# Optimization experiments

Measured on AMD Instinct MI355X. Metric: run time of the kernel, lower is better.

The kernel has to match this reference:

```python
import jax, jax.numpy as jnp
from jax import lax
import numpy as np

B, N, S, K = 8, 4096, 1024, 32
D_FEAT = 64
EPS = 1e-5


def fps_idx(pts, npoint):
    # pts: [N,3] -> farthest point sampling indices [npoint] (deterministic start at 0)
    n = pts.shape[0]
    def body(i, state):
        dist, far, idxs = state
        idxs = idxs.at[i].set(far)
        d = jnp.sum((pts - pts[far]) ** 2, axis=-1)
        dist = jnp.minimum(dist, d)
        return dist, jnp.argmax(dist).astype(jnp.int32), idxs
    init = (jnp.full((n,), 1e10, pts.dtype), jnp.int32(0), jnp.zeros((npoint,), jnp.int32))
    _, _, idxs = lax.fori_loop(0, npoint, body, init)
    return idxs


def bn(x, g, b, axes, c_axis):
    # batch-norm, training mode (batch statistics), matching torch default module state
    m = jnp.mean(x, axes, keepdims=True)
    v = jnp.var(x, axes, keepdims=True)
    shape = [1] * x.ndim
    shape[c_axis] = -1
    return g.reshape(shape) * (x - m) * lax.rsqrt(v + EPS) + b.reshape(shape)


def conv1x1(x, w, b):
    # x: [B,C,S,K], w: [O,C], b: [O]
    return jnp.einsum('oc,bcsk->bosk', w, x) + b[None, :, None, None]


def setup_inputs():
    key = jax.random.key(0)
    ks = jax.random.split(key, 20)
    p = lambda k, shape: jax.random.normal(k, shape, jnp.float32) * 0.05
    inp = {
        'xyz': jax.random.normal(ks[0], (B, 3, N), jnp.float32),
        'features': jax.random.normal(ks[1], (B, D_FEAT, N), jnp.float32),
        # main MLP: 67 -> 64 -> 64 -> 128
        'w0': p(ks[2], (64, 67)), 'b0': p(ks[3], (64,)), 'g0': jnp.ones(64), 'be0': jnp.zeros(64),
        'w1': p(ks[4], (64, 64)), 'b1': p(ks[5], (64,)), 'g1': jnp.ones(64), 'be1': jnp.zeros(64),
        'w2': p(ks[6], (128, 64)), 'b2': p(ks[7], (128,)), 'g2': jnp.ones(128), 'be2': jnp.zeros(128),
        # WeightNet: 3 -> 8 -> 8 -> 16
        'ww0': p(ks[8], (8, 3)), 'wb0': p(ks[9], (8,)), 'wg0': jnp.ones(8), 'wbe0': jnp.zeros(8),
        'ww1': p(ks[10], (8, 8)), 'wb1': p(ks[11], (8,)), 'wg1': jnp.ones(8), 'wbe1': jnp.zeros(8),
        'ww2': p(ks[12], (16, 8)), 'wb2': p(ks[13], (16,)), 'wg2': jnp.ones(16), 'wbe2': jnp.zeros(16),
        # final linear 16*128 -> 128 and BN1d
        'lw': p(ks[14], (128, 16 * 128)), 'lb': p(ks[15], (128,)),
        'lg': jnp.ones(128), 'lbe': jnp.zeros(128),
    }
    return inp


def reference(xyz, features, w0, b0, g0, be0, w1, b1, g1, be1, w2, b2, g2, be2,
              ww0, wb0, wg0, wbe0, ww1, wb1, wg1, wbe1, ww2, wb2, wg2, wbe2,
              lw, lb, lg, lbe):
    xyz_t = jnp.transpose(xyz, (0, 2, 1))          # [B,N,3]
    feat_t = jnp.transpose(features, (0, 2, 1))    # [B,N,D]

    # farthest point sampling (indices non-differentiable, as in CUDA FPS)
    fidx = jax.vmap(lambda pts: fps_idx(pts, S))(lax.stop_gradient(xyz_t))  # [B,S]
    fps_xyz = jnp.take_along_axis(xyz_t, fidx[..., None], axis=1)           # [B,S,3]

    # KNN: squared distances [B,S,N], take K smallest
    d2 = (jnp.sum(fps_xyz ** 2, -1, keepdims=True)
          + jnp.sum(xyz_t ** 2, -1)[:, None, :]
          - 2.0 * jnp.einsum('bsc,bnc->bsn', fps_xyz, xyz_t))
    _, idx = lax.top_k(-lax.stop_gradient(d2), K)                            # [B,S,K]

    gather = jax.vmap(lambda src, i: src[i])
    grouped_xyz = gather(xyz_t, idx) - fps_xyz[:, :, None, :]                # [B,S,K,3]
    grouped_feat = gather(feat_t, idx)                                       # [B,S,K,D]
    nf = jnp.concatenate([grouped_xyz, grouped_feat], axis=-1)               # [B,S,K,3+D]

    nf = jnp.transpose(nf, (0, 3, 1, 2))                                     # [B,C,S,K]
    for w, b, g, be in ((w0, b0, g0, be0), (w1, b1, g1, be1), (w2, b2, g2, be2)):
        nf = jax.nn.relu(bn(conv1x1(nf, w, b), g, be, (0, 2, 3), 1))

    gx = jnp.transpose(grouped_xyz, (0, 3, 1, 2))                            # [B,3,S,K]
    wts = gx
    for w, b, g, be in ((ww0, wb0, wg0, wbe0), (ww1, wb1, wg1, wbe1), (ww2, wb2, wg2, wbe2)):
        wts = jax.nn.relu(bn(conv1x1(wts, w, b), g, be, (0, 2, 3), 1))       # [B,16,S,K]

    agg = jnp.einsum('bdsk,bcsk->bsdc', nf, wts)                             # [B,S,128,16]
    agg = agg.reshape(agg.shape[0], agg.shape[1], -1)                        # [B,S,2048] (D outer, C inner)
    lin = agg @ lw.T + lb                                                    # [B,S,128]
    lin = jnp.transpose(lin, (0, 2, 1))                                      # [B,128,S]
    out_f = jax.nn.relu(bn(lin, lg, lbe, (0, 2), 1))

    new_xyz = jnp.transpose(fps_xyz, (0, 2, 1))                              # [B,3,S]
    return (new_xyz, out_f)
```

## Files before the change

kernel.cpp:

```cpp
#include <hip/hip_runtime.h>
#include <hip/hip_bf16.h>

#define BB 8
#define NN 4096
#define SS 1024
#define KK 32
#define PP (BB*SS*KK)

typedef unsigned long long u64;
typedef unsigned int u32;
typedef unsigned short u16;
typedef float f32x2 __attribute__((ext_vector_type(2)));

#define ST_Y0 0
#define ST_W0 64
#define ST_Y1 72
#define ST_W1 136
#define ST_Y2 144
#define ST_W2 272
#define ST_LIN 288

static __device__ __forceinline__ float bf2f(u32 u){ return __uint_as_float(u<<16); }
static __device__ __forceinline__ u16 f2bf(float f){ u32 u=__float_as_uint(f); return (u16)((u + 0x7FFFu + ((u>>16)&1u))>>16); }

static __device__ __forceinline__ f32x2 pk_add(f32x2 a, f32x2 b){
  f32x2 d; asm("v_pk_add_f32 %0, %1, %2" : "=v"(d) : "v"(a), "v"(b)); return d;
}
static __device__ __forceinline__ f32x2 pk_mul(f32x2 a, f32x2 b){
  f32x2 d; asm("v_pk_mul_f32 %0, %1, %2" : "=v"(d) : "v"(a), "v"(b)); return d;
}

static __device__ __forceinline__ uint4 pack8(const float* v){
  uint4 r;
  r.x=(u32)f2bf(v[0])|((u32)f2bf(v[1])<<16);
  r.y=(u32)f2bf(v[2])|((u32)f2bf(v[3])<<16);
  r.z=(u32)f2bf(v[4])|((u32)f2bf(v[5])<<16);
  r.w=(u32)f2bf(v[6])|((u32)f2bf(v[7])<<16);
  return r;
}

static __device__ __forceinline__ void unp8_aff(uint4 r, const float* A, const float* C, int cb, float* o){
  o[0]=fmaxf(fmaf(bf2f(r.x&0xffffu),A[cb+0],C[cb+0]),0.f);
  o[1]=fmaxf(fmaf(bf2f(r.x>>16)    ,A[cb+1],C[cb+1]),0.f);
  o[2]=fmaxf(fmaf(bf2f(r.y&0xffffu),A[cb+2],C[cb+2]),0.f);
  o[3]=fmaxf(fmaf(bf2f(r.y>>16)    ,A[cb+3],C[cb+3]),0.f);
  o[4]=fmaxf(fmaf(bf2f(r.z&0xffffu),A[cb+4],C[cb+4]),0.f);
  o[5]=fmaxf(fmaf(bf2f(r.z>>16)    ,A[cb+5],C[cb+5]),0.f);
  o[6]=fmaxf(fmaf(bf2f(r.w&0xffffu),A[cb+6],C[cb+6]),0.f);
  o[7]=fmaxf(fmaf(bf2f(r.w>>16)    ,A[cb+7],C[cb+7]),0.f);
}

template<int CTRL, int RMASK>
static __device__ __forceinline__ u32 dppmax(u32 m){
  u32 t=(u32)__builtin_amdgcn_update_dpp(0, (int)m, CTRL, RMASK, 0xf, false);
  return t>m ? t : m;
}
template<int CTRL, int RMASK>
static __device__ __forceinline__ float dppadd1(float v){
  float t=__uint_as_float((u32)__builtin_amdgcn_update_dpp(0,(int)__float_as_uint(v),CTRL,RMASK,0xf,false));
  return v+t;
}
static __device__ __forceinline__ float dppsum(float v){
  v=dppadd1<0x111,0xf>(v);
  v=dppadd1<0x112,0xf>(v);
  v=dppadd1<0x114,0xf>(v);
  v=dppadd1<0x118,0xf>(v);
  v=dppadd1<0x142,0xa>(v);
  v=dppadd1<0x143,0xc>(v);
  return v;
}
static __device__ __forceinline__ float rl63(float v){
  return __uint_as_float((u32)__builtin_amdgcn_readlane((int)__float_as_uint(v),63));
}

__global__ __launch_bounds__(256) void k_featT(const float* __restrict__ f, float* __restrict__ ft,
    const float* __restrict__ w0,const float* __restrict__ w1,const float* __restrict__ w2,
    const float* __restrict__ ww0,const float* __restrict__ ww1,const float* __restrict__ ww2,
    float* __restrict__ w0t,float* __restrict__ w1t,float* __restrict__ w2t,
    float* __restrict__ wt0,float* __restrict__ wt1,float* __restrict__ wt2,
    float* __restrict__ statsf){
  __shared__ float tile[64][65];
  if (blockIdx.x==512){
    int t=threadIdx.x;
    for (int i=t;i<1024;i+=256) statsf[i]=0.f;
    for (int i=t;i<64*67;i+=256){ int o=i/67,k=i%67; w0t[k*64+o]=w0[i]; }
    for (int i=t;i<64*64;i+=256){ int o=i>>6,k=i&63; w1t[k*64+o]=w1[i]; }
    for (int i=t;i<128*64;i+=256){ int o=i>>6,k=i&63; w2t[k*128+o]=w2[i]; }
    for (int i=t;i<8*3;i+=256){ int o=i/3,k=i%3; wt0[k*8+o]=ww0[i]; }
    for (int i=t;i<8*8;i+=256){ int o=i>>3,k=i&7; wt1[k*8+o]=ww1[i]; }
    for (int i=t;i<16*8;i+=256){ int o=i>>3,k=i&7; wt2[k*16+o]=ww2[i]; }
    return;
  }
  int b=blockIdx.x>>6; int n0=(blockIdx.x&63)*64;
  const float* fb=f+(size_t)b*64*NN;
  int c0=threadIdx.x>>6, nn=threadIdx.x&63;
  #pragma unroll
  for (int it=0;it<16;it++){ int c=c0+it*4; tile[c][nn]=fb[(size_t)c*NN+n0+nn]; }
  __syncthreads();
  int cc=threadIdx.x&63, n1=threadIdx.x>>6;
  float* fo=ft+((size_t)b*NN+n0)*64;
  #pragma unroll
  for (int it=0;it<16;it++){ int n=n1+it*4; fo[(size_t)n*64+cc]=tile[cc][n]; }
}

__global__ __launch_bounds__(512) void k_fps(const float* __restrict__ xyz,
                                             float* __restrict__ fpsq, float* __restrict__ outx){
  __shared__ float X[NN], Y[NN], Z[NN];
  __shared__ float QX[SS], QY[SS], QZ[SS];
  __shared__ u64 red[2][8];
  int b=blockIdx.x, t=threadIdx.x;
  const float* xb=xyz+(size_t)b*3*NN;
  for (int i=t;i<NN;i+=512){ X[i]=xb[i]; Y[i]=xb[NN+i]; Z[i]=xb[2*NN+i]; }
  __syncthreads();
  f32x2 px[4],py[4],pz[4],dd[4];
  #pragma unroll
  for (int k=0;k<4;k++){
    int i=t*8+2*k;
    px[k].x=X[i]; px[k].y=X[i+1];
    py[k].x=Y[i]; py[k].y=Y[i+1];
    pz[k].x=Z[i]; pz[k].y=Z[i+1];
    dd[k].x=1e10f; dd[k].y=1e10f;
  }
  int wv=t>>6, ln=t&63;
  int far=0;
  for (int s=0;s<SS;s++){
    float fx=X[far], fy=Y[far], fz=Z[far];
    if (t==0){ QX[s]=fx; QY[s]=fy; QZ[s]=fz; }
    f32x2 nfx, nfy, nfz;
    nfx.x=-fx; nfx.y=-fx; nfy.x=-fy; nfy.y=-fy; nfz.x=-fz; nfz.y=-fz;
    #pragma unroll
    for (int k=0;k<4;k++){
      f32x2 dx=pk_add(px[k],nfx);
      f32x2 xx=pk_mul(dx,dx);
      f32x2 dy=pk_add(py[k],nfy);
      f32x2 yy=pk_mul(dy,dy);
      f32x2 dz=pk_add(pz[k],nfz);
      f32x2 zz=pk_mul(dz,dz);
      f32x2 s1=pk_add(xx,yy);
      f32x2 d2=pk_add(s1,zz);
      dd[k].x=fminf(dd[k].x,d2.x);
      dd[k].y=fminf(dd[k].y,d2.y);
    }
    float m01=fmaxf(dd[0].x,dd[0].y), m23=fmaxf(dd[1].x,dd[1].y);
    float m45=fmaxf(dd[2].x,dd[2].y), m67=fmaxf(dd[3].x,dd[3].y);
    u32 m=__float_as_uint(fmaxf(fmaxf(m01,m23),fmaxf(m45,m67)));
    m=dppmax<0x111,0xf>(m);
    m=dppmax<0x112,0xf>(m);
    m=dppmax<0x114,0xf>(m);
    m=dppmax<0x118,0xf>(m);
    u32 r15=(u32)__builtin_amdgcn_readlane((int)m,15);
    u32 r31=(u32)__builtin_amdgcn_readlane((int)m,31);
    u32 r47=(u32)__builtin_amdgcn_readlane((int)m,47);
    u32 r63=(u32)__builtin_amdgcn_readlane((int)m,63);
    u32 ab = r15>r31 ? r15 : r31;
    u32 cd = r47>r63 ? r47 : r63;
    u32 wmax = ab>cd ? ab : cd;
    int lj=8;
    if (__float_as_uint(dd[3].y)==wmax) lj=7;
    if (__float_as_uint(dd[3].x)==wmax) lj=6;
    if (__float_as_uint(dd[2].y)==wmax) lj=5;
    if (__float_as_uint(dd[2].x)==wmax) lj=4;
    if (__float_as_uint(dd[1].y)==wmax) lj=3;
    if (__float_as_uint(dd[1].x)==wmax) lj=2;
    if (__float_as_uint(dd[0].y)==wmax) lj=1;
    if (__float_as_uint(dd[0].x)==wmax) lj=0;
    u64 ball=__ballot(lj<8);
    u32 wl=(u32)__builtin_ctzll(ball);
    int gi=t*8+lj;
    u32 widx=(u32)__builtin_amdgcn_readlane(gi,wl);
    int pb=s&1;
    if (ln==0) red[pb][wv]=((u64)wmax<<32)|(u32)(4095u-widx);
    __syncthreads();
    const double* rd=(const double*)&red[pb][0];
    double g=fmax(fmax(fmax(rd[0],rd[1]),fmax(rd[2],rd[3])),
                  fmax(fmax(rd[4],rd[5]),fmax(rd[6],rd[7])));
    far=4095-(int)(__double_as_longlong(g)&0xFFFull);
  }
  __syncthreads();
  for (int i=t;i<SS;i+=512){
    float qx=QX[i], qy=QY[i], qz=QZ[i];
    float* q=&fpsq[((size_t)b*SS+i)*3]; q[0]=qx; q[1]=qy; q[2]=qz;
    outx[b*3*SS+i]=qx; outx[b*3*SS+SS+i]=qy; outx[b*3*SS+2*SS+i]=qz;
  }
}

#define KSTR 68
__global__ __launch_bounds__(256) void k_knn(const float* __restrict__ xyz, const float* __restrict__ fpsq,
                                             int* __restrict__ kidx){
  extern __shared__ char smem[];
  float* xs=(float*)smem;
  float* ys=xs+64*KSTR;
  float* zs=ys+64*KSTR;
  float* pn=zs+64*KSTR;
  int blk=blockIdx.x; int b=blk>>8; int s0=(blk&255)*4;
  const float* xb=xyz+(size_t)b*3*NN;
  for (int i=threadIdx.x;i<NN;i+=256){
    float x=xb[i],y=xb[NN+i],z=xb[2*NN+i];
    int slot=(i>>6)*KSTR+(i&63);
    xs[slot]=x; ys[slot]=y; zs[slot]=z;
    pn[slot]=__fadd_rn(__fadd_rn(__fmul_rn(x,x),__fmul_rn(y,y)),__fmul_rn(z,z));
  }
  __syncthreads();
  int wv=threadIdx.x>>6, ln=threadIdx.x&63;
  int s=s0+wv;
  const float* q=&fpsq[((size_t)b*SS+s)*3];
  float qx=q[0],qy=q[1],qz=q[2];
  float qn=__fadd_rn(__fadd_rn(__fmul_rn(qx,qx),__fmul_rn(qy,qy)),__fmul_rn(qz,qz));
  f32x2 qxx,qyy,qzz,qnn,mtwo;
  qxx.x=qx;qxx.y=qx; qyy.x=qy;qyy.y=qy; qzz.x=qz;qzz.y=qz; qnn.x=qn;qnn.y=qn;
  mtwo.x=-2.f; mtwo.y=-2.f;
  const float4* Xp=(const float4*)(xs+ln*KSTR);
  const float4* Yp=(const float4*)(ys+ln*KSTR);
  const float4* Zp=(const float4*)(zs+ln*KSTR);
  const float4* Pp=(const float4*)(pn+ln*KSTR);
  int base=ln*64;
  u64 v[64];
  #pragma unroll
  for (int g=0;g<16;g++){
    float4 x4=Xp[g], y4=Yp[g], z4=Zp[g], p4=Pp[g];
    #pragma unroll
    for (int h=0;h<2;h++){
      f32x2 px2,py2,pz2,pn2;
      if (h==0){ px2.x=x4.x;px2.y=x4.y; py2.x=y4.x;py2.y=y4.y; pz2.x=z4.x;pz2.y=z4.y; pn2.x=p4.x;pn2.y=p4.y; }
      else     { px2.x=x4.z;px2.y=x4.w; py2.x=y4.z;py2.y=y4.w; pz2.x=z4.z;pz2.y=z4.w; pn2.x=p4.z;pn2.y=p4.w; }
      f32x2 m1=pk_mul(qxx,px2);
      f32x2 mm=pk_mul(qyy,py2);
      f32x2 a1=pk_add(m1,mm);
      f32x2 m3=pk_mul(qzz,pz2);
      f32x2 dt=pk_add(a1,m3);
      f32x2 qp=pk_add(qnn,pn2);
      f32x2 nd=pk_mul(dt,mtwo);
      f32x2 d2=pk_add(qp,nd);
      #pragma unroll
      for (int e=0;e<2;e++){
        u32 bu=__float_as_uint(e?d2.y:d2.x);
        bu = ((int)bu<0)? ~bu : (bu|0x80000000u);
        v[g*4+h*2+e]=((u64)bu<<32)|(u32)(base+g*4+h*2+e);
      }
    }
  }
  u64 cand[8];
  #pragma unroll
  for (int gg=0;gg<8;gg++){
    u64 c=v[gg*8];
    #pragma unroll
    for (int j=1;j<8;j++){ u64 x=v[gg*8+j]; c = x<c?x:c; }
    cand[gg]=c;
  }
  u64 best=cand[0];
  #pragma unroll
  for (int gg=1;gg<8;gg++){ u64 x=cand[gg]; best = x<best?x:best; }
  int my=0;
  #pragma unroll 1
  for (int r=0;r<KK;r++){
    u64 w=best;
    #pragma unroll
    for (int m=1;m<64;m<<=1){ u64 o=__shfl_xor(w,m,64); w = o<w?o:w; }
    if (ln==r) my=(int)(w&0xFFFull);
    if (best==w){
      #pragma unroll
      for (int gg=0;gg<8;gg++){
        if (cand[gg]==w){
          u64 c=~0ull;
          #pragma unroll
          for (int j=0;j<8;j++){ u64 x=v[gg*8+j]; x = x>w ? x : ~0ull; c = x<c?x:c; }
          cand[gg]=c;
        }
      }
      u64 nb=cand[0];
      #pragma unroll
      for (int gg=1;gg<8;gg++){ u64 x=cand[gg]; nb = x<nb?x:nb; }
      best=nb;
    }
  }
  if (ln<KK) kidx[(((size_t)b*SS+s)<<5)+ln]=my;
}

__global__ __launch_bounds__(256) void k_l0(const float* __restrict__ xyz, const float* __restrict__ ft,
    const float* __restrict__ fpsq, const int* __restrict__ kidx,
    const float* __restrict__ w0t, const float* __restrict__ wt0,
    u16* __restrict__ y0, float* __restrict__ wl0, float* __restrict__ statsf){
  __shared__ u16 ytile[256][64];
  __shared__ float pS[4][64], pQ[4][64];
  __shared__ float pWS[4][8], pWQ[4][8];
  int t=threadIdx.x; int wv=t>>6, ln=t&63;
  int p=blockIdx.x*256+t;
  int b=p>>15;
  int site=p>>5;
  int j=kidx[p];
  const float* xb=xyz+(size_t)b*3*NN;
  const float* q=fpsq+(size_t)site*3;
  float gx=xb[j]-q[0], gy=xb[NN+j]-q[1], gz=xb[2*NN+j]-q[2];
  float acc[64];
  #pragma unroll
  for (int c=0;c<64;c++) acc[c]=fmaf(gx,w0t[c],fmaf(gy,w0t[64+c],gz*w0t[128+c]));
  const float4* fr=(const float4*)(ft+((size_t)b*NN+j)*64);
  #pragma unroll 1
  for (int kb=0;kb<4;kb++){
    float4 r0=fr[kb*4+0], r1=fr[kb*4+1], r2=fr[kb*4+2], r3=fr[kb*4+3];
    float ch[16]={r0.x,r0.y,r0.z,r0.w,r1.x,r1.y,r1.z,r1.w,r2.x,r2.y,r2.z,r2.w,r3.x,r3.y,r3.z,r3.w};
    const float* wb=w0t+(3+kb*16)*64;
    #pragma unroll
    for (int kk=0;kk<16;kk++){
      #pragma unroll
      for (int c=0;c<64;c++) acc[c]=fmaf(ch[kk],wb[kk*64+c],acc[c]);
    }
  }
  u16* yr=y0+(size_t)p*64;
  #pragma unroll
  for (int c8=0;c8<8;c8++){
    uint4 pk=pack8(&acc[c8*8]);
    ((uint4*)yr)[c8]=pk;
    *((uint4*)&ytile[t][c8*8])=pk;
  }
  float wa[8];
  #pragma unroll
  for (int o=0;o<8;o++) wa[o]=fmaf(gx,wt0[o],fmaf(gy,wt0[8+o],gz*wt0[16+o]));
  float4* wr=(float4*)(wl0+(size_t)p*8);
  wr[0]=make_float4(wa[0],wa[1],wa[2],wa[3]);
  wr[1]=make_float4(wa[4],wa[5],wa[6],wa[7]);
  float wS[8],wQ[8];
  #pragma unroll
  for (int o=0;o<8;o++){
    wS[o]=rl63(dppsum(wa[o]));
    wQ[o]=rl63(dppsum(wa[o]*wa[o]));
  }
  if (ln==0){
    #pragma unroll
    for (int o=0;o<8;o++){ pWS[wv][o]=wS[o]; pWQ[wv][o]=wQ[o]; }
  }
  __syncthreads();
  {
    int c=t&63, rg=t>>6;
    float S=0.f,Q=0.f;
    #pragma unroll 16
    for (int r=0;r<64;r++){
      float v=bf2f((u32)ytile[rg*64+r][c]);
      S+=v; Q=fmaf(v,v,Q);
    }
    pS[rg][c]=S; pQ[rg][c]=Q;
  }
  __syncthreads();
  if (t<64){
    float S=pS[0][t]+pS[1][t]+pS[2][t]+pS[3][t];
    float Q=pQ[0][t]+pQ[1][t]+pQ[2][t]+pQ[3][t];
    atomicAdd(&statsf[2*(ST_Y0+t)],S); atomicAdd(&statsf[2*(ST_Y0+t)+1],Q);
  } else if (t<72){
    int c=t-64;
    float S=pWS[0][c]+pWS[1][c]+pWS[2][c]+pWS[3][c];
    float Q=pWQ[0][c]+pWQ[1][c]+pWQ[2][c]+pWQ[3][c];
    atomicAdd(&statsf[2*(ST_W0+c)],S); atomicAdd(&statsf[2*(ST_W0+c)+1],Q);
  }
}

__global__ __launch_bounds__(256) void k_l1(const u16* __restrict__ y0, const float* __restrict__ wl0,
    const float* __restrict__ w1t, const float* __restrict__ wt1,
    const float* __restrict__ statsf,
    const float* __restrict__ g0v, const float* __restrict__ be0v,
    const float* __restrict__ wg0v, const float* __restrict__ wbe0v,
    u16* __restrict__ y1, float* __restrict__ wl1, float* __restrict__ statso){
  __shared__ float A0[64],C0[64],AW[8],CW[8];
  __shared__ u16 ytile[256][64];
  __shared__ float pS[4][64], pQ[4][64];
  __shared__ float pWS[4][8], pWQ[4][8];
  int t=threadIdx.x; int wv=t>>6, ln=t&63;
  if (t<64){
    float sm=statsf[(ST_Y0+t)*2], sq=statsf[(ST_Y0+t)*2+1];
    float mean=sm*(1.f/PP), var=fmaxf(sq*(1.f/PP)-mean*mean,0.f);
    float a=g0v[t]*rsqrtf(var+1e-5f); A0[t]=a; C0[t]=be0v[t]-mean*a;
  } else if (t<72){
    int c=t-64;
    float sm=statsf[(ST_W0+c)*2], sq=statsf[(ST_W0+c)*2+1];
    float mean=sm*(1.f/PP), var=fmaxf(sq*(1.f/PP)-mean*mean,0.f);
    float a=wg0v[c]*rsqrtf(var+1e-5f); AW[c]=a; CW[c]=wbe0v[c]-mean*a;
  }
  __syncthreads();
  int p=blockIdx.x*256+t;
  const uint4* yr=(const uint4*)(y0+(size_t)p*64);
  float acc[64];
  #pragma unroll
  for (int c=0;c<64;c++) acc[c]=0.f;
  #pragma unroll 1
  for (int kb=0;kb<4;kb++){
    uint4 r0=yr[kb*2], r1=yr[kb*2+1];
    float ch[16];
    unp8_aff(r0,A0,C0,kb*16,ch);
    unp8_aff(r1,A0,C0,kb*16+8,ch+8);
    const float* wb=w1t+kb*16*64;
    #pragma unroll
    for (int kk=0;kk<16;kk++){
      #pragma unroll
      for (int c=0;c<64;c++) acc[c]=fmaf(ch[kk],wb[kk*64+c],acc[c]);
    }
  }
  u16* yo=y1+(size_t)p*64;
  #pragma unroll
  for (int c8=0;c8<8;c8++){
    uint4 pk=pack8(&acc[c8*8]);
    ((uint4*)yo)[c8]=pk;
    *((uint4*)&ytile[t][c8*8])=pk;
  }
  const float4* wvp=(const float4*)(wl0+(size_t)p*8);
  float4 v0=wvp[0], v1=wvp[1];
  float wi[8]={v0.x,v0.y,v0.z,v0.w,v1.x,v1.y,v1.z,v1.w};
  float wo[8];
  #pragma unroll
  for (int o=0;o<8;o++) wo[o]=0.f;
  #pragma unroll
  for (int k=0;k<8;k++){
    float xr=fmaxf(fmaf(wi[k],AW[k],CW[k]),0.f);
    #pragma unroll
    for (int o=0;o<8;o++) wo[o]=fmaf(xr,wt1[k*8+o],wo[o]);
  }
  float4* wr=(float4*)(wl1+(size_t)p*8);
  wr[0]=make_float4(wo[0],wo[1],wo[2],wo[3]);
  wr[1]=make_float4(wo[4],wo[5],wo[6],wo[7]);
  float wS[8],wQ[8];
  #pragma unroll
  for (int o=0;o<8;o++){
    wS[o]=rl63(dppsum(wo[o]));
    wQ[o]=rl63(dppsum(wo[o]*wo[o]));
  }
  if (ln==0){
    #pragma unroll
    for (int o=0;o<8;o++){ pWS[wv][o]=wS[o]; pWQ[wv][o]=wQ[o]; }
  }
  __syncthreads();
  {
    int c=t&63, rg=t>>6;
    float S=0.f,Q=0.f;
    #pragma unroll 16
    for (int r=0;r<64;r++){
      float v=bf2f((u32)ytile[rg*64+r][c]);
      S+=v; Q=fmaf(v,v,Q);
    }
    pS[rg][c]=S; pQ[rg][c]=Q;
  }
  __syncthreads();
  if (t<64){
    float S=pS[0][t]+pS[1][t]+pS[2][t]+pS[3][t];
    float Q=pQ[0][t]+pQ[1][t]+pQ[2][t]+pQ[3][t];
    atomicAdd(&statso[2*(ST_Y1+t)],S); atomicAdd(&statso[2*(ST_Y1+t)+1],Q);
  } else if (t<72){
    int c=t-64;
    float S=pWS[0][c]+pWS[1][c]+pWS[2][c]+pWS[3][c];
    float Q=pWQ[0][c]+pWQ[1][c]+pWQ[2][c]+pWQ[3][c];
    atomicAdd(&statso[2*(ST_W1+c)],S); atomicAdd(&statso[2*(ST_W1+c)+1],Q);
  }
}

__global__ __launch_bounds__(256) void k_l2(const u16* __restrict__ y1, const float* __restrict__ wl1,
    const float* __restrict__ w2t, const float* __restrict__ wt2,
    const float* __restrict__ statsf,
    const float* __restrict__ g1v, const float* __restrict__ be1v,
    const float* __restrict__ wg1v, const float* __restrict__ wbe1v,
    u16* __restrict__ y2, float* __restrict__ wl2, float* __restrict__ statso){
  __shared__ float A1[64],C1[64],AW[8],CW[8];
  __shared__ u16 ytile[256][64];
  __shared__ float pS[4][64], pQ[4][64];
  __shared__ float pWS[4][16], pWQ[4][16];
  int t=threadIdx.x; int wv=t>>6, ln=t&63;
  if (t<64){
    float sm=statsf[(ST_Y1+t)*2], sq=statsf[(ST_Y1+t)*2+1];
    float mean=sm*(1.f/PP), var=fmaxf(sq*(1.f/PP)-mean*mean,0.f);
    float a=g1v[t]*rsqrtf(var+1e-5f); A1[t]=a; C1[t]=be1v[t]-mean*a;
  } else if (t<72){
    int c=t-64;
    float sm=statsf[(ST_W1+c)*2], sq=statsf[(ST_W1+c)*2+1];
    float mean=sm*(1.f/PP), var=fmaxf(sq*(1.f/PP)-mean*mean,0.f);
    float a=wg1v[c]*rsqrtf(var+1e-5f); AW[c]=a; CW[c]=wbe1v[c]-mean*a;
  }
  __syncthreads();
  int p=blockIdx.x*256+t;
  const uint4* yr=(const uint4*)(y1+(size_t)p*64);
  #pragma unroll 1
  for (int h=0;h<2;h++){
    float acc[64];
    #pragma unroll
    for (int c=0;c<64;c++) acc[c]=0.f;
    #pragma unroll 1
    for (int kb=0;kb<4;kb++){
      uint4 r0=yr[kb*2], r1=yr[kb*2+1];
      float ch[16];
      unp8_aff(r0,A1,C1,kb*16,ch);
      unp8_aff(r1,A1,C1,kb*16+8,ch+8);
      const float* wb=w2t+(size_t)kb*16*128+h*64;
      #pragma unroll
      for (int kk=0;kk<16;kk++){
        #pragma unroll
        for (int c=0;c<64;c++) acc[c]=fmaf(ch[kk],wb[kk*128+c],acc[c]);
      }
    }
    u16* yo=y2+(size_t)p*128+h*64;
    #pragma unroll
    for (int c8=0;c8<8;c8++){
      uint4 pk=pack8(&acc[c8*8]);
      ((uint4*)yo)[c8]=pk;
      *((uint4*)&ytile[t][c8*8])=pk;
    }
    __syncthreads();
    {
      int c=t&63, rg=t>>6;
      float S=0.f,Q=0.f;
      #pragma unroll 16
      for (int r=0;r<64;r++){
        float v=bf2f((u32)ytile[rg*64+r][c]);
        S+=v; Q=fmaf(v,v,Q);
      }
      pS[rg][c]=S; pQ[rg][c]=Q;
    }
    __syncthreads();
    if (t<64){
      float S=pS[0][t]+pS[1][t]+pS[2][t]+pS[3][t];
      float Q=pQ[0][t]+pQ[1][t]+pQ[2][t]+pQ[3][t];
      atomicAdd(&statso[2*(ST_Y2+h*64+t)],S); atomicAdd(&statso[2*(ST_Y2+h*64+t)+1],Q);
    }
    __syncthreads();
  }
  const float4* wvp=(const float4*)(wl1+(size_t)p*8);
  float4 v0=wvp[0], v1=wvp[1];
  float wi[8]={v0.x,v0.y,v0.z,v0.w,v1.x,v1.y,v1.z,v1.w};
  float wo[16];
  #pragma unroll
  for (int o=0;o<16;o++) wo[o]=0.f;
  #pragma unroll
  for (int k=0;k<8;k++){
    float xr=fmaxf(fmaf(wi[k],AW[k],CW[k]),0.f);
    #pragma unroll
    for (int o=0;o<16;o++) wo[o]=fmaf(xr,wt2[k*16+o],wo[o]);
  }
  float4* wr=(float4*)(wl2+(size_t)p*16);
  wr[0]=make_float4(wo[0],wo[1],wo[2],wo[3]);
  wr[1]=make_float4(wo[4],wo[5],wo[6],wo[7]);
  wr[2]=make_float4(wo[8],wo[9],wo[10],wo[11]);
  wr[3]=make_float4(wo[12],wo[13],wo[14],wo[15]);
  float wS[16],wQ[16];
  #pragma unroll
  for (int o=0;o<16;o++){
    wS[o]=rl63(dppsum(wo[o]));
    wQ[o]=rl63(dppsum(wo[o]*wo[o]));
  }
  if (ln==0){
    #pragma unroll
    for (int o=0;o<16;o++){ pWS[wv][o]=wS[o]; pWQ[wv][o]=wQ[o]; }
  }
  __syncthreads();
  if (t<16){
    float S=pWS[0][t]+pWS[1][t]+pWS[2][t]+pWS[3][t];
    float Q=pWQ[0][t]+pWQ[1][t]+pWQ[2][t]+pWQ[3][t];
    atomicAdd(&statso[2*(ST_W2+t)],S); atomicAdd(&statso[2*(ST_W2+t)+1],Q);
  }
}

__global__ __launch_bounds__(256) void k_agg(const u16* __restrict__ y2, const float* __restrict__ wl2,
    const float* __restrict__ statsf,
    const float* __restrict__ g2v, const float* __restrict__ be2v,
    const float* __restrict__ wg2v, const float* __restrict__ wbe2v,
    u16* __restrict__ agg){
  __shared__ float A2[128],C2[128],AW[16],CW[16];
  __shared__ float nf[32*128];
  __shared__ float wt[32*16];
  int site=blockIdx.x; int t=threadIdx.x;
  if (t<128){
    float sm=statsf[(ST_Y2+t)*2], sq=statsf[(ST_Y2+t)*2+1];
    float mean=sm*(1.f/PP), var=fmaxf(sq*(1.f/PP)-mean*mean,0.f);
    float a=g2v[t]*rsqrtf(var+1e-5f); A2[t]=a; C2[t]=be2v[t]-mean*a;
  } else if (t<144){
    int c=t-128;
    float sm=statsf[(ST_W2+c)*2], sq=statsf[(ST_W2+c)*2+1];
    float mean=sm*(1.f/PP), var=fmaxf(sq*(1.f/PP)-mean*mean,0.f);
    float a=wg2v[c]*rsqrtf(var+1e-5f); AW[c]=a; CW[c]=wbe2v[c]-mean*a;
  }
  __syncthreads();
  const uint4* src=(const uint4*)(y2+(size_t)site*32*128);
  #pragma unroll
  for (int it=0;it<2;it++){
    int idx=t+it*256;
    uint4 r=src[idx];
    int base=(idx*8)&127; int kq=(idx*8)>>7;
    unp8_aff(r,A2,C2,base,&nf[kq*128+base]);
  }
  #pragma unroll
  for (int it=0;it<2;it++){
    int i=t+it*256;
    float x=wl2[(size_t)site*512+i]; int c=i&15;
    wt[i]=fmaxf(fmaf(x,AW[c],CW[c]),0.f);
  }
  __syncthreads();
  int d=t>>1, cb=(t&1)*8;
  float acc[8];
  #pragma unroll
  for (int e=0;e<8;e++) acc[e]=0.f;
  #pragma unroll 4
  for (int kq=0;kq<32;kq++){
    float nv=nf[kq*128+d];
    #pragma unroll
    for (int e=0;e<8;e++) acc[e]=fmaf(nv,wt[kq*16+cb+e],acc[e]);
  }
  ((uint4*)(agg+(size_t)site*2048))[t]=pack8(acc);
}

__global__ __launch_bounds__(256) void k_lin(const u16* __restrict__ agg, const float* __restrict__ lw,
                                             float* __restrict__ lin, float* __restrict__ outst){
  __shared__ float As[32][33];
  __shared__ float Bs[32][128];
  __shared__ float stS[8][132], stQ[8][132];
  int s0=blockIdx.x*32; int t=threadIdx.x;
  int tx=t&31, ty=t>>5;
  float acc[4][4];
  #pragma unroll
  for (int i=0;i<4;i++){
    #pragma unroll
    for (int jj=0;jj<4;jj++) acc[i][jj]=0.f;
  }
  for (int kb=0;kb<2048;kb+=32){
    {
      int row=t>>3, kc=(t&7)*4;
      uint2 raw=*(const uint2*)(agg+((size_t)(s0+row))*2048+kb+kc);
      As[row][kc  ]=bf2f(raw.x&0xffffu); As[row][kc+1]=bf2f(raw.x>>16);
      As[row][kc+2]=bf2f(raw.y&0xffffu); As[row][kc+3]=bf2f(raw.y>>16);
    }
    {
      int o=t>>1, ks=(t&1)*16;
      const float* lr=lw+(size_t)o*2048+kb+ks;
      #pragma unroll
      for (int i=0;i<16;i+=4){
        float4 r=*(const float4*)(lr+i);
        Bs[ks+i][o]=r.x; Bs[ks+i+1][o]=r.y; Bs[ks+i+2][o]=r.z; Bs[ks+i+3][o]=r.w;
      }
    }
    __syncthreads();
    #pragma unroll 8
    for (int kk=0;kk<32;kk++){
      float av[4];
      #pragma unroll
      for (int i=0;i<4;i++) av[i]=As[ty*4+i][kk];
      float4 bv=*(const float4*)(&Bs[kk][tx*4]);
      #pragma unroll
      for (int i=0;i<4;i++){
        acc[i][0]=fmaf(av[i],bv.x,acc[i][0]);
        acc[i][1]=fmaf(av[i],bv.y,acc[i][1]);
        acc[i][2]=fmaf(av[i],bv.z,acc[i][2]);
        acc[i][3]=fmaf(av[i],bv.w,acc[i][3]);
      }
    }
    __syncthreads();
  }
  #pragma unroll
  for (int i=0;i<4;i++){
    float4 o4=make_float4(acc[i][0],acc[i][1],acc[i][2],acc[i][3]);
    *(float4*)(lin+((size_t)(s0+ty*4+i))*128+tx*4)=o4;
  }
  #pragma unroll
  for (int jj=0;jj<4;jj++){
    float a0=acc[0][jj],a1=acc[1][jj],a2=acc[2][jj],a3=acc[3][jj];
    stS[ty][tx*4+jj]=(a0+a1)+(a2+a3);
    stQ[ty][tx*4+jj]=fmaf(a3,a3,fmaf(a2,a2,fmaf(a1,a1,a0*a0)));
  }
  __syncthreads();
  if (t<128){
    float S=0.f,Q=0.f;
    #pragma unroll
    for (int k=0;k<8;k++){ S+=stS[k][t]; Q+=stQ[k][t]; }
    atomicAdd(&outst[2*t],S); atomicAdd(&outst[2*t+1],Q);
  }
}

__global__ __launch_bounds__(256) void k_out(const float* __restrict__ lin, const float* __restrict__ statsf,
    const float* __restrict__ lg, const float* __restrict__ lbe, float* __restrict__ outf){
  int t=blockIdx.x*256+threadIdx.x;
  int s4=(t&255)*4; int o=(t>>8)&127; int b=t>>15;
  float sm=statsf[(ST_LIN+o)*2], sq=statsf[(ST_LIN+o)*2+1];
  float mean=sm*(1.f/8192.f), var=fmaxf(sq*(1.f/8192.f)-mean*mean,0.f);
  float a=lg[o]*rsqrtf(var+1e-5f), cc=lbe[o]-mean*a;
  float v0=lin[((size_t)b*SS+s4+0)*128+o];
  float v1=lin[((size_t)b*SS+s4+1)*128+o];
  float v2=lin[((size_t)b*SS+s4+2)*128+o];
  float v3=lin[((size_t)b*SS+s4+3)*128+o];
  float4 r=make_float4(fmaxf(fmaf(v0,a,cc),0.f),fmaxf(fmaf(v1,a,cc),0.f),
                       fmaxf(fmaf(v2,a,cc),0.f),fmaxf(fmaf(v3,a,cc),0.f));
  *(float4*)(outf+((size_t)b*128+o)*SS+s4)=r;
}

extern "C" void kernel_launch(void* const* d_in, const int* in_sizes, int n_in,
                              void* d_out, int out_size, void* d_ws, size_t ws_size,
                              hipStream_t stream){
  (void)in_sizes;(void)n_in;(void)out_size;(void)ws_size;
  const float* xyz =(const float*)d_in[0];
  const float* feat=(const float*)d_in[1];
  const float* w0=(const float*)d_in[2];  const float* g0=(const float*)d_in[4];  const float* be0=(const float*)d_in[5];
  const float* w1=(const float*)d_in[6];  const float* g1=(const float*)d_in[8];  const float* be1=(const float*)d_in[9];
  const float* w2=(const float*)d_in[10]; const float* g2=(const float*)d_in[12]; const float* be2=(const float*)d_in[13];
  const float* ww0=(const float*)d_in[14]; const float* wg0=(const float*)d_in[16]; const float* wbe0=(const float*)d_in[17];
  const float* ww1=(const float*)d_in[18]; const float* wg1=(const float*)d_in[20]; const float* wbe1=(const float*)d_in[21];
  const float* ww2=(const float*)d_in[22]; const float* wg2=(const float*)d_in[24]; const float* wbe2=(const float*)d_in[25];
  const float* lw=(const float*)d_in[26]; const float* lg=(const float*)d_in[28]; const float* lbe=(const float*)d_in[29];
  float* out=(float*)d_out;
  char* ws=(char*)d_ws;

  size_t cur=0;
  auto alloc=[&](size_t bytes)->size_t{ cur=(cur+255)&~(size_t)255; size_t o=cur; cur+=bytes; return o; };
  size_t o_stats=alloc(4096);
  size_t o_w0t =alloc(67*64*4);
  size_t o_w1t =alloc(64*64*4);
  size_t o_w2t =alloc(64*128*4);
  size_t o_wt0 =alloc(3*8*4);
  size_t o_wt1 =alloc(8*8*4);
  size_t o_wt2 =alloc(8*16*4);
  size_t o_fpsq=alloc((size_t)BB*SS*3*4);
  size_t o_kidx=alloc((size_t)PP*4);
  size_t o_ft  =alloc((size_t)BB*NN*64*4);
  size_t o_y0  =alloc((size_t)PP*64*2);
  size_t o_y1  =alloc((size_t)PP*64*2);
  size_t o_y2  =alloc((size_t)PP*128*2);
  size_t o_wl0 =alloc((size_t)PP*8*4);
  size_t o_wl1 =alloc((size_t)PP*8*4);
  size_t o_wl2 =alloc((size_t)PP*16*4);
  size_t o_agg =alloc((size_t)8192*2048*2);
  size_t o_lin =alloc((size_t)8192*128*4);

  float* statsf=(float*)(ws+o_stats);
  float* w0t=(float*)(ws+o_w0t); float* w1t=(float*)(ws+o_w1t); float* w2t=(float*)(ws+o_w2t);
  float* wt0=(float*)(ws+o_wt0); float* wt1=(float*)(ws+o_wt1); float* wt2=(float*)(ws+o_wt2);
  float* fpsq=(float*)(ws+o_fpsq); int* kidx=(int*)(ws+o_kidx);
  float* ft=(float*)(ws+o_ft);
  u16* y0=(u16*)(ws+o_y0); u16* y1=(u16*)(ws+o_y1); u16* y2=(u16*)(ws+o_y2);
  float* wl0=(float*)(ws+o_wl0); float* wl1=(float*)(ws+o_wl1); float* wl2=(float*)(ws+o_wl2);
  u16* agg=(u16*)(ws+o_agg); float* lin=(float*)(ws+o_lin);

  size_t knn_smem = (size_t)4*64*KSTR*4;

  hipLaunchKernelGGL(k_featT,dim3(513),dim3(256),0,stream,feat,ft,
                     w0,w1,w2,ww0,ww1,ww2,w0t,w1t,w2t,wt0,wt1,wt2,statsf);
  hipLaunchKernelGGL(k_fps,dim3(BB),dim3(512),0,stream,xyz,fpsq,out);
  hipLaunchKernelGGL(k_knn,dim3(2048),dim3(256),knn_smem,stream,xyz,fpsq,kidx);
  hipLaunchKernelGGL(k_l0,dim3(PP/256),dim3(256),0,stream,xyz,ft,fpsq,kidx,w0t,wt0,y0,wl0,statsf);
  hipLaunchKernelGGL(k_l1,dim3(PP/256),dim3(256),0,stream,y0,wl0,w1t,wt1,statsf,g0,be0,wg0,wbe0,y1,wl1,statsf);
  hipLaunchKernelGGL(k_l2,dim3(PP/256),dim3(256),0,stream,y1,wl1,w2t,wt2,statsf,g1,be1,wg1,wbe1,y2,wl2,statsf);
  hipLaunchKernelGGL(k_agg,dim3(8192),dim3(256),0,stream,y2,wl2,statsf,g2,be2,wg2,wbe2,agg);
  hipLaunchKernelGGL(k_lin,dim3(256),dim3(256),0,stream,agg,lw,lin,statsf+2*ST_LIN);
  hipLaunchKernelGGL(k_out,dim3(1024),dim3(256),0,stream,lin,statsf,lg,lbe,out+BB*3*SS);
}
```

Baseline: 1.308 ms.

## Merge feature transpose and weight prep into FPS kernel to overlap with FPS

Fuses the feature-transpose/weight-transpose kernel into the FPS kernel launch. Blocks 0-7 run FPS, blocks 8-263 transpose feature tiles (two tiles per 512-thread block), and block 264 zeroes stats and transposes weights. Shared memory is a union of the FPS arrays and the transpose tiles. This hides the transpose work under the latency-bound serial FPS loop and removes one launch, but every block now reserves the larger FPS shared-memory footprint, which may limit how many transpose blocks run at once.

```diff
diff --git a/kernel.cpp b/kernel.cpp
--- a/kernel.cpp
+++ b/kernel.cpp
@@ -73,42 +73,47 @@
   return __uint_as_float((u32)__builtin_amdgcn_readlane((int)__float_as_uint(v),63));
 }
 
-__global__ __launch_bounds__(256) void k_featT(const float* __restrict__ f, float* __restrict__ ft,
+__global__ __launch_bounds__(512) void k_fps_ft(const float* __restrict__ xyz,
+    float* __restrict__ fpsq, float* __restrict__ outx,
+    const float* __restrict__ f, float* __restrict__ ft,
     const float* __restrict__ w0,const float* __restrict__ w1,const float* __restrict__ w2,
     const float* __restrict__ ww0,const float* __restrict__ ww1,const float* __restrict__ ww2,
     float* __restrict__ w0t,float* __restrict__ w1t,float* __restrict__ w2t,
     float* __restrict__ wt0,float* __restrict__ wt1,float* __restrict__ wt2,
     float* __restrict__ statsf){
-  __shared__ float tile[64][65];
-  if (blockIdx.x==512){
-    int t=threadIdx.x;
-    for (int i=t;i<1024;i+=256) statsf[i]=0.f;
-    for (int i=t;i<64*67;i+=256){ int o=i/67,k=i%67; w0t[k*64+o]=w0[i]; }
-    for (int i=t;i<64*64;i+=256){ int o=i>>6,k=i&63; w1t[k*64+o]=w1[i]; }
-    for (int i=t;i<128*64;i+=256){ int o=i>>6,k=i&63; w2t[k*128+o]=w2[i]; }
-    for (int i=t;i<8*3;i+=256){ int o=i/3,k=i%3; wt0[k*8+o]=ww0[i]; }
-    for (int i=t;i<8*8;i+=256){ int o=i>>3,k=i&7; wt1[k*8+o]=ww1[i]; }
-    for (int i=t;i<16*8;i+=256){ int o=i>>3,k=i&7; wt2[k*16+o]=ww2[i]; }
+  __shared__ union USm {
+    struct { float X[NN],Y[NN],Z[NN]; float QX[SS],QY[SS],QZ[SS]; u64 red[2][8]; } a;
+    float tile[2][64][65];
+  } sm;
+  int blk=blockIdx.x; int t=threadIdx.x;
+  if (blk>=8){
+    if (blk==264){
+      for (int i=t;i<1024;i+=512) statsf[i]=0.f;
+      for (int i=t;i<64*67;i+=512){ int o=i/67,k=i%67; w0t[k*64+o]=w0[i]; }
+      for (int i=t;i<64*64;i+=512){ int o=i>>6,k=i&63; w1t[k*64+o]=w1[i]; }
+      for (int i=t;i<128*64;i+=512){ int o=i>>6,k=i&63; w2t[k*128+o]=w2[i]; }
+      for (int i=t;i<8*3;i+=512){ int o=i/3,k=i%3; wt0[k*8+o]=ww0[i]; }
+      for (int i=t;i<8*8;i+=512){ int o=i>>3,k=i&7; wt1[k*8+o]=ww1[i]; }
+      for (int i=t;i<16*8;i+=512){ int o=i>>3,k=i&7; wt2[k*16+o]=ww2[i]; }
+      return;
+    }
+    int sub=t>>8, tt=t&255;
+    int tileIdx=(blk-8)*2+sub;
+    int b=tileIdx>>6; int n0=(tileIdx&63)*64;
+    const float* fb=f+(size_t)b*64*NN;
+    int c0=tt>>6, nn=tt&63;
+    #pragma unroll
+    for (int it=0;it<16;it++){ int c=c0+it*4; sm.tile[sub][c][nn]=fb[(size_t)c*NN+n0+nn]; }
+    __syncthreads();
+    int cc=tt&63, n1=tt>>6;
+    float* fo=ft+((size_t)b*NN+n0)*64;
+    #pragma unroll
+    for (int it=0;it<16;it++){ int n=n1+it*4; fo[(size_t)n*64+cc]=sm.tile[sub][cc][n]; }
     return;
   }
-  int b=blockIdx.x>>6; int n0=(blockIdx.x&63)*64;
-  const float* fb=f+(size_t)b*64*NN;
-  int c0=threadIdx.x>>6, nn=threadIdx.x&63;
-  #pragma unroll
-  for (int it=0;it<16;it++){ int c=c0+it*4; tile[c][nn]=fb[(size_t)c*NN+n0+nn]; }
-  __syncthreads();
-  int cc=threadIdx.x&63, n1=threadIdx.x>>6;
-  float* fo=ft+((size_t)b*NN+n0)*64;
-  #pragma unroll
-  for (int it=0;it<16;it++){ int n=n1+it*4; fo[(size_t)n*64+cc]=tile[cc][n]; }
-}
-
-__global__ __launch_bounds__(512) void k_fps(const float* __restrict__ xyz,
-                                             float* __restrict__ fpsq, float* __restrict__ outx){
-  __shared__ float X[NN], Y[NN], Z[NN];
-  __shared__ float QX[SS], QY[SS], QZ[SS];
-  __shared__ u64 red[2][8];
-  int b=blockIdx.x, t=threadIdx.x;
+  float* X=sm.a.X; float* Y=sm.a.Y; float* Z=sm.a.Z;
+  float* QX=sm.a.QX; float* QY=sm.a.QY; float* QZ=sm.a.QZ;
+  int b=blk;
   const float* xb=xyz+(size_t)b*3*NN;
   for (int i=t;i<NN;i+=512){ X[i]=xb[i]; Y[i]=xb[NN+i]; Z[i]=xb[2*NN+i]; }
   __syncthreads();
@@ -169,9 +174,9 @@
     int gi=t*8+lj;
     u32 widx=(u32)__builtin_amdgcn_readlane(gi,wl);
     int pb=s&1;
-    if (ln==0) red[pb][wv]=((u64)wmax<<32)|(u32)(4095u-widx);
+    if (ln==0) sm.a.red[pb][wv]=((u64)wmax<<32)|(u32)(4095u-widx);
     __syncthreads();
-    const double* rd=(const double*)&red[pb][0];
+    const double* rd=(const double*)&sm.a.red[pb][0];
     double g=fmax(fmax(fmax(rd[0],rd[1]),fmax(rd[2],rd[3])),
                   fmax(fmax(rd[4],rd[5]),fmax(rd[6],rd[7])));
     far=4095-(int)(__double_as_longlong(g)&0xFFFull);
@@ -730,9 +735,8 @@
 
   size_t knn_smem = (size_t)4*64*KSTR*4;
 
-  hipLaunchKernelGGL(k_featT,dim3(513),dim3(256),0,stream,feat,ft,
+  hipLaunchKernelGGL(k_fps_ft,dim3(265),dim3(512),0,stream,xyz,fpsq,out,feat,ft,
                      w0,w1,w2,ww0,ww1,ww2,w0t,w1t,w2t,wt0,wt1,wt2,statsf);
-  hipLaunchKernelGGL(k_fps,dim3(BB),dim3(512),0,stream,xyz,fpsq,out);
   hipLaunchKernelGGL(k_knn,dim3(2048),dim3(256),knn_smem,stream,xyz,fpsq,kidx);
   hipLaunchKernelGGL(k_l0,dim3(PP/256),dim3(256),0,stream,xyz,ft,fpsq,kidx,w0t,wt0,y0,wl0,statsf);
   hipLaunchKernelGGL(k_l1,dim3(PP/256),dim3(256),0,stream,y0,wl0,w1t,wt1,statsf,g0,be0,wg0,wbe0,y1,wl1,statsf);
```

New measurement: 1.315 ms. Within noise of the previous version (+0.5%).
